# Kernel tuning notes

Hardware: AMD Instinct MI355X
Metric: run time of the kernel (lower is better)

Reference implementation:

```python
import jax, jax.numpy as jnp
import numpy as np

D_MODEL = 512
NUM_HEADS = 8
D_HEAD = D_MODEL // NUM_HEADS
QMAX = 127.0  # int8 narrow-range symmetric
EPS = 1e-8


def _quant_dequant_weight(w):
    # per-output-channel symmetric int8 quant-dequant (brevitas default style)
    s = jnp.maximum(jnp.max(jnp.abs(w), axis=1, keepdims=True) / QMAX, EPS)
    return jnp.clip(jnp.round(w / s), -QMAX, QMAX) * s


def _quant_dequant_act(x):
    # per-tensor symmetric int8 quant-dequant (QuantIdentity)
    s = jnp.maximum(jnp.max(jnp.abs(x)) / QMAX, EPS)
    return jnp.clip(jnp.round(x / s), -QMAX, QMAX) * s


def _qlinear(x, w, b):
    return jnp.einsum('btd,od->bto', x, _quant_dequant_weight(w)) + b


def setup_inputs() -> dict:
    key = jax.random.key(0)
    ks = jax.random.split(key, 10)
    B, T = 2, 4096
    lim = 1.0 / np.sqrt(D_MODEL)
    mk = lambda k: jax.random.uniform(k, (D_MODEL, D_MODEL), jnp.float32, -lim, lim)
    mb = lambda k: jax.random.uniform(k, (D_MODEL,), jnp.float32, -lim, lim)
    return {
        'x': jax.random.normal(ks[0], (B, T, D_MODEL), jnp.float32),
        'mask': jax.random.randint(ks[1], (B, T), 0, 2, jnp.int32),
        'Wq': mk(ks[2]), 'bq': mb(ks[3]),
        'Wk': mk(ks[4]), 'bk': mb(ks[5]),
        'Wv': mk(ks[6]), 'bv': mb(ks[7]),
        'Wo': mk(ks[8]), 'bo': mb(ks[9]),
    }


def reference(x, mask, Wq, bq, Wk, bk, Wv, bv, Wo, bo):
    B, T, _ = x.shape
    shape = lambda t: t.reshape(B, T, NUM_HEADS, D_HEAD).transpose(0, 2, 1, 3)  # (B,H,T,dh)
    q = shape(_qlinear(x, Wq, bq))
    k = shape(_qlinear(x, Wk, bk))
    v = shape(_qlinear(x, Wv, bv))
    scores = jnp.einsum('bhtd,bhsd->bhts', q, k) / np.sqrt(D_HEAD)
    keep = (mask != 0)[:, None, None, :]  # (B,1,1,T), 0 = masked
    scores = jnp.where(keep, scores, -jnp.inf)
    attn = jax.nn.softmax(scores, axis=-1)
    ctx = jnp.einsum('bhts,bhsd->bhtd', attn, v)
    ctx = ctx.transpose(0, 2, 1, 3).reshape(B, T, D_MODEL)
    out = _qlinear(ctx, Wo, bo)
    return _quant_dequant_act(out)
```

## Files before the change

### kernel.cpp

```cpp
#include <hip/hip_runtime.h>
#include <hip/hip_bf16.h>

typedef __bf16 bf16;
typedef __bf16 bf16x8 __attribute__((ext_vector_type(8)));
typedef __bf16 bf16x4v __attribute__((ext_vector_type(4)));
typedef float f32x4 __attribute__((ext_vector_type(4)));

#define D_MODEL 512
#define T_SEQ   4096
#define NH      8
#define DH      64
#define M_ROWS  8192
#define VROW    8224
#define QK_SCALE 0.18033688011112042f

__device__ __forceinline__ void gload16(const void* g, void* l) {
  __builtin_amdgcn_global_load_lds(
      (const __attribute__((address_space(1))) unsigned int*)g,
      (__attribute__((address_space(3))) unsigned int*)l, 16, 0, 0);
}

#define WAITV(N) asm volatile("s_waitcnt vmcnt(" #N ")" ::: "memory")
#define CFENCE   asm volatile("" ::: "memory")

__global__ __launch_bounds__(256) void prep_all(
    const void* __restrict__ x, const int* __restrict__ mask,
    const void* __restrict__ Wq, const void* __restrict__ Wk,
    const void* __restrict__ Wv, const void* __restrict__ Wo,
    const void* __restrict__ bq, const void* __restrict__ bk,
    const void* __restrict__ bv, const void* __restrict__ bo,
    bf16* __restrict__ out, float* __restrict__ bf, float* __restrict__ mf,
    int* __restrict__ flag, unsigned int* __restrict__ amax)
{
  __shared__ int wcnt[4];
  __shared__ int sfl;
  const int tid = threadIdx.x;
  const unsigned short* xr = (const unsigned short*)x;

  int cnt = 0;
  for (int i = tid; i < 4096; i += 256) {
    unsigned short u = xr[i];
    int e = (u >> 7) & 0xFF;
    bool insane = (e >= 133) || (e > 0 && e <= 96) || (e == 0 && (u & 0x7F) != 0);
    cnt += insane ? 1 : 0;
  }
#pragma unroll
  for (int off = 32; off >= 1; off >>= 1) cnt += __shfl_xor(cnt, off);
  if ((tid & 63) == 0) wcnt[tid >> 6] = cnt;
  __syncthreads();
  if (tid == 0) sfl = ((wcnt[0] + wcnt[1] + wcnt[2] + wcnt[3]) > 400) ? 1 : 0;
  __syncthreads();
  const int fl = sfl;

  const int blk = blockIdx.x;
  if (blk < 512) {
    int wave = tid >> 6, lane = tid & 63;
    int gid = blk * 4 + wave;
    int w = gid >> 9, row = gid & 511;
    const void* W = (w == 0) ? Wq : (w == 1) ? Wk : (w == 2) ? Wv : Wo;
    float v[8]; float am = 0.f;
#pragma unroll
    for (int i = 0; i < 8; i++) {
      int idx = row * D_MODEL + lane + 64 * i;
      v[i] = fl ? ((const float*)W)[idx] : (float)((const bf16*)W)[idx];
      am = fmaxf(am, fabsf(v[i]));
    }
#pragma unroll
    for (int off = 32; off >= 1; off >>= 1) am = fmaxf(am, __shfl_xor(am, off));
    float s = fmaxf(am / 127.0f, 1e-8f);
    bf16* dst = out + (size_t)gid * D_MODEL;
#pragma unroll
    for (int i = 0; i < 8; i++) {
      float q = rintf(v[i] / s);
      q = fminf(fmaxf(q, -127.f), 127.f);
      dst[lane + 64 * i] = (bf16)(q * s);
    }
  } else {
    int ab = blk - 512;
    int j = ab * 1024 + tid * 4;
    int4 mv = *(const int4*)&mask[j];
    mf[j + 0] = mv.x ? -16.0f : -1e30f;
    mf[j + 1] = mv.y ? -16.0f : -1e30f;
    mf[j + 2] = mv.z ? -16.0f : -1e30f;
    mf[j + 3] = mv.w ? -16.0f : -1e30f;
    if (ab == 0) {
      const void* ps[4] = {bq, bk, bv, bo};
      for (int t = tid; t < 4 * D_MODEL; t += 256) {
        int w = t >> 9, o = t & 511;
        bf[t] = fl ? ((const float*)ps[w])[o] : (float)((const bf16*)ps[w])[o];
      }
      if (tid == 0) { *flag = fl; *amax = 0u; }
    }
  }
}

__global__ __launch_bounds__(256) void convert_x(const void* __restrict__ xr,
                                                 const int* __restrict__ flag,
                                                 bf16* __restrict__ xb, int n)
{
  int i = (blockIdx.x * blockDim.x + threadIdx.x) * 4;
  if (i >= n) return;
  if (*flag) {
    float4 v = *(const float4*)((const float*)xr + i);
    __align__(8) bf16 o[4] = {(bf16)v.x, (bf16)v.y, (bf16)v.z, (bf16)v.w};
    *(uint2*)(xb + i) = *(uint2*)o;
  } else {
    *(uint2*)(xb + i) = *(const uint2*)((const bf16*)xr + i);
  }
}

__global__ __launch_bounds__(256) void gemm_qkv(
    const bf16* __restrict__ A, const bf16* __restrict__ W,
    const float* __restrict__ bias,
    bf16* __restrict__ Qh, bf16* __restrict__ Kh, bf16* __restrict__ VTP)
{
  __shared__ __align__(16) bf16 As[2][128 * 32];
  __shared__ __align__(16) bf16 Bs[2][128 * 32];

  const int tid = threadIdx.x;
  const int wave = tid >> 6, lane = tid & 63;
  const int lr = lane & 15, quad = lane >> 4;
  const int wm = (wave >> 1) * 64, wn = (wave & 1) * 64;
  const int m0 = blockIdx.x * 128, n0 = blockIdx.y * 128;
  const int sec = blockIdx.y >> 2;

  const bf16* aSrc[2]; const bf16* bSrc[2];
#pragma unroll
  for (int ii = 0; ii < 2; ii++) {
    int s = ii * 256 + tid, row = s >> 2, sl = s & 3;
    int g = (row ^ (row >> 2)) & 3;
    aSrc[ii] = A + (size_t)(m0 + row) * D_MODEL + ((sl ^ g) << 3);
    bSrc[ii] = W + (size_t)(n0 + row) * D_MODEL + ((sl ^ g) << 3);
  }

  f32x4 acc[4][4];
#pragma unroll
  for (int i = 0; i < 4; i++)
#pragma unroll
    for (int j = 0; j < 4; j++) acc[i][j] = f32x4{0.f, 0.f, 0.f, 0.f};

#pragma unroll
  for (int d = 0; d < 2; d++) {
#pragma unroll
    for (int ii = 0; ii < 2; ii++) {
      int s = ii * 256 + tid;
      gload16(aSrc[ii] + d * 32, &As[d][s * 8]);
      gload16(bSrc[ii] + d * 32, &Bs[d][s * 8]);
    }
  }
  WAITV(4);
  __builtin_amdgcn_s_barrier();
  CFENCE;

  for (int k = 0; k < 16; k++) {
    const int cur = k & 1;
    bf16x8 af[4], bfr[4];
#pragma unroll
    for (int mt = 0; mt < 4; mt++) {
      int row = wm + mt * 16 + lr;
      af[mt] = *(const bf16x8*)&As[cur][row * 32 + ((quad ^ ((row ^ (row >> 2)) & 3)) << 3)];
    }
#pragma unroll
    for (int nt = 0; nt < 4; nt++) {
      int row = wn + nt * 16 + lr;
      bfr[nt] = *(const bf16x8*)&Bs[cur][row * 32 + ((quad ^ ((row ^ (row >> 2)) & 3)) << 3)];
    }
    if (sec == 2) {
#pragma unroll
      for (int mt = 0; mt < 4; mt++)
#pragma unroll
        for (int nt = 0; nt < 4; nt++)
          acc[mt][nt] = __builtin_amdgcn_mfma_f32_16x16x32_bf16(af[mt], bfr[nt], acc[mt][nt], 0, 0, 0);
    } else {
#pragma unroll
      for (int mt = 0; mt < 4; mt++)
#pragma unroll
        for (int nt = 0; nt < 4; nt++)
          acc[nt][mt] = __builtin_amdgcn_mfma_f32_16x16x32_bf16(bfr[nt], af[mt], acc[nt][mt], 0, 0, 0);
    }

    if (k < 15) {
      __builtin_amdgcn_s_barrier();
      CFENCE;
      if (k < 14) {
#pragma unroll
        for (int ii = 0; ii < 2; ii++) {
          int s = ii * 256 + tid;
          gload16(aSrc[ii] + (k + 2) * 32, &As[cur][s * 8]);
          gload16(bSrc[ii] + (k + 2) * 32, &Bs[cur][s * 8]);
        }
        WAITV(4);
      } else {
        WAITV(0);
      }
      __builtin_amdgcn_s_barrier();
      CFENCE;
    }
  }

  if (sec == 2) {
#pragma unroll
    for (int mt = 0; mt < 4; mt++) {
      int grow = m0 + wm + mt * 16 + quad * 4;
#pragma unroll
      for (int nt = 0; nt < 4; nt++) {
        int gcol = n0 + wn + nt * 16 + lr;
        float b = bias[gcol];
        bf16x4v pk;
#pragma unroll
        for (int r = 0; r < 4; r++) pk[r] = (bf16)(acc[mt][nt][r] + b);
        *(bf16x4v*)(VTP + (size_t)(gcol - 1024) * VROW + grow) = pk;
      }
    }
  } else {
    const float scale = (sec == 0) ? QK_SCALE : 1.0f;
    bf16* dst = (sec == 0) ? Qh : Kh;
#pragma unroll
    for (int i = 0; i < 4; i++) {
      int cbase = n0 + wn + i * 16 + quad * 4;
      int c = cbase & 511;
      int hh = c >> 6, c64 = c & 63;
      f32x4 bv = *(const f32x4*)&bias[cbase];
#pragma unroll
      for (int j = 0; j < 4; j++) {
        int row = m0 + wm + j * 16 + lr;
        int bb = row >> 12, t = row & 4095;
        bf16x4v pk;
#pragma unroll
        for (int r = 0; r < 4; r++) pk[r] = (bf16)((acc[i][j][r] + bv[r]) * scale);
        *(bf16x4v*)(dst + ((size_t)(bb * NH + hh) * T_SEQ + t) * DH + c64) = pk;
      }
    }
  }
}

__global__ __launch_bounds__(256) void gemm_o(
    const bf16* __restrict__ A, const bf16* __restrict__ W,
    const float* __restrict__ bias,
    float* __restrict__ Cf, unsigned int* __restrict__ amaxp)
{
  __shared__ __align__(16) bf16 As[2][64 * 32];
  __shared__ __align__(16) bf16 Bs[2][128 * 32];
  __shared__ float wred[4];

  const int tid = threadIdx.x;
  const int wave = tid >> 6, lane = tid & 63;
  const int lr = lane & 15, quad = lane >> 4;
  const int wm = (wave >> 1) * 32, wn = (wave & 1) * 64;
  const int m0 = blockIdx.x * 64, n0 = blockIdx.y * 128;

  const bf16* aSrc; const bf16* bSrc[2];
  {
    int s = tid, row = s >> 2, sl = s & 3;
    int g = (row ^ (row >> 2)) & 3;
    aSrc = A + (size_t)(m0 + row) * D_MODEL + ((sl ^ g) << 3);
  }
#pragma unroll
  for (int ii = 0; ii < 2; ii++) {
    int s = ii * 256 + tid, row = s >> 2, sl = s & 3;
    int g = (row ^ (row >> 2)) & 3;
    bSrc[ii] = W + (size_t)(n0 + row) * D_MODEL + ((sl ^ g) << 3);
  }

  f32x4 acc[2][4];
#pragma unroll
  for (int i = 0; i < 2; i++)
#pragma unroll
    for (int j = 0; j < 4; j++) acc[i][j] = f32x4{0.f, 0.f, 0.f, 0.f};

#pragma unroll
  for (int d = 0; d < 2; d++) {
    gload16(aSrc + d * 32, &As[d][tid * 8]);
#pragma unroll
    for (int ii = 0; ii < 2; ii++) {
      int s = ii * 256 + tid;
      gload16(bSrc[ii] + d * 32, &Bs[d][s * 8]);
    }
  }
  WAITV(3);
  __builtin_amdgcn_s_barrier();
  CFENCE;

  for (int k = 0; k < 16; k++) {
    const int cur = k & 1;
    bf16x8 af[2], bfr[4];
#pragma unroll
    for (int mt = 0; mt < 2; mt++) {
      int row = wm + mt * 16 + lr;
      af[mt] = *(const bf16x8*)&As[cur][row * 32 + ((quad ^ ((row ^ (row >> 2)) & 3)) << 3)];
    }
#pragma unroll
    for (int nt = 0; nt < 4; nt++) {
      int row = wn + nt * 16 + lr;
      bfr[nt] = *(const bf16x8*)&Bs[cur][row * 32 + ((quad ^ ((row ^ (row >> 2)) & 3)) << 3)];
    }
#pragma unroll
    for (int mt = 0; mt < 2; mt++)
#pragma unroll
      for (int nt = 0; nt < 4; nt++)
        acc[mt][nt] = __builtin_amdgcn_mfma_f32_16x16x32_bf16(af[mt], bfr[nt], acc[mt][nt], 0, 0, 0);

    if (k < 15) {
      __builtin_amdgcn_s_barrier();
      CFENCE;
      if (k < 14) {
        gload16(aSrc + (k + 2) * 32, &As[cur][tid * 8]);
#pragma unroll
        for (int ii = 0; ii < 2; ii++) {
          int s = ii * 256 + tid;
          gload16(bSrc[ii] + (k + 2) * 32, &Bs[cur][s * 8]);
        }
        WAITV(3);
      } else {
        WAITV(0);
      }
      __builtin_amdgcn_s_barrier();
      CFENCE;
    }
  }

  float lmax = 0.f;
#pragma unroll
  for (int mt = 0; mt < 2; mt++) {
    int grow = m0 + wm + mt * 16 + quad * 4;
#pragma unroll
    for (int nt = 0; nt < 4; nt++) {
      int gcol = n0 + wn + nt * 16 + lr;
      float b = bias[gcol];
#pragma unroll
      for (int r = 0; r < 4; r++) {
        float v = acc[mt][nt][r] + b;
        Cf[(size_t)(grow + r) * D_MODEL + gcol] = v;
        lmax = fmaxf(lmax, fabsf(v));
      }
    }
  }
#pragma unroll
  for (int off = 32; off >= 1; off >>= 1) lmax = fmaxf(lmax, __shfl_xor(lmax, off));
  if (lane == 0) wred[wave] = lmax;
  __syncthreads();
  if (tid == 0) {
    float m = fmaxf(fmaxf(wred[0], wred[1]), fmaxf(wred[2], wred[3]));
    atomicMax(amaxp, __float_as_uint(m));
  }
}

__global__ __launch_bounds__(256, 2) void attn(
    const bf16* __restrict__ Q, const bf16* __restrict__ K, const bf16* __restrict__ VT,
    const float* __restrict__ maskf, bf16* __restrict__ ctx)
{
  __shared__ __align__(16) bf16 Ks[3][64 * 64];
  __shared__ __align__(16) bf16 Vs[3][64 * 64];
  __shared__ __align__(16) float Mf[T_SEQ];

  const int tid = threadIdx.x;
  const int wave = tid >> 6, lane = tid & 63;
  const int lr = lane & 15, quad = lane >> 4;
  const int i = blockIdx.x;
  const int bh = (i & 7) * 2 + ((i >> 3) & 1);
  const int qb = i >> 4;
  const int b = bh >> 3, h = bh & 7;
  const int q0 = qb * 128 + wave * 32;

  const bf16* Qb = Q + (size_t)bh * T_SEQ * DH;
  const bf16* Kb = K + (size_t)bh * T_SEQ * DH;
  const bf16* Vb = VT + (size_t)(h * DH) * VROW + (size_t)b * T_SEQ;
  const float* mb = maskf + b * T_SEQ;

  const int phase = (qb * 2) & 63;

  const bf16* kSrc[2]; const bf16* vSrc[2];
#pragma unroll
  for (int ii = 0; ii < 2; ii++) {
    int s = ii * 256 + tid, row = s >> 3, sl = s & 7;
    int kt = row >> 4, m = row & 15;
    int keym = ((m >> 2) << 3) + ((kt & 1) << 2) + (m & 3) + ((kt >> 1) << 5);
    kSrc[ii] = Kb + (size_t)keym * DH + ((sl ^ (row & 7)) << 3);
    vSrc[ii] = Vb + (size_t)row * VROW + ((sl ^ (row & 7)) << 3);
  }

  bf16x8 qf[2][2];
#pragma unroll
  for (int qt = 0; qt < 2; qt++) {
    const bf16* rq = Qb + (size_t)(q0 + qt * 16 + lr) * DH;
    qf[qt][0] = *(const bf16x8*)(rq + quad * 8);
    qf[qt][1] = *(const bf16x8*)(rq + 32 + quad * 8);
  }
  WAITV(0);

#pragma unroll
  for (int ii = 0; ii < 4; ii++) {
    int g = ii * 256 + tid;
    gload16(mb + g * 4, &Mf[g * 4]);
  }
#pragma unroll
  for (int d = 0; d < 3; d++) {
    int kb = ((phase + d) & 63) * 64;
#pragma unroll
    for (int ii = 0; ii < 2; ii++) {
      int s = ii * 256 + tid;
      gload16(kSrc[ii] + (size_t)kb * DH, &Ks[d][s * 8]);
      gload16(vSrc[ii] + kb, &Vs[d][s * 8]);
    }
  }

  f32x4 O[2][4];
#pragma unroll
  for (int a = 0; a < 2; a++)
#pragma unroll
    for (int c = 0; c < 4; c++) O[a][c] = f32x4{0.f, 0.f, 0.f, 0.f};
  float lacc[2] = {0.f, 0.f};

  WAITV(8);
  __builtin_amdgcn_s_barrier();
  CFENCE;

  int cur = 0, cc = phase;
  for (int j = 0; j < 64; j++) {
    f32x4 mk[4];
#pragma unroll
    for (int kt = 0; kt < 4; kt++)
      mk[kt] = *(const f32x4*)&Mf[cc * 64 + ((kt >> 1) << 5) + (quad << 3) + ((kt & 1) << 2)];

    bf16x8 kr[4][2];
#pragma unroll
    for (int kt = 0; kt < 4; kt++)
#pragma unroll
      for (int kh = 0; kh < 2; kh++)
        kr[kt][kh] = *(const bf16x8*)&Ks[cur][(kt * 16 + lr) * 64 +
                                             (((kh * 4 + quad) ^ (lr & 7)) << 3)];

    bf16x8 pfa[2][2];
#pragma unroll
    for (int qt = 0; qt < 2; qt++) {
      f32x4 z[4];
#pragma unroll
      for (int kt = 0; kt < 4; kt++) {
        f32x4 t = mk[kt];
        t = __builtin_amdgcn_mfma_f32_16x16x32_bf16(kr[kt][0], qf[qt][0], t, 0, 0, 0);
        t = __builtin_amdgcn_mfma_f32_16x16x32_bf16(kr[kt][1], qf[qt][1], t, 0, 0, 0);
        z[kt] = t;
      }
      float la = lacc[qt];
#pragma unroll
      for (int kt = 0; kt < 4; kt++) {
#pragma unroll
        for (int r = 0; r < 4; r++) {
          float p = __builtin_amdgcn_exp2f(z[kt][r]);
          la += p;
          pfa[qt][kt >> 1][((kt & 1) << 2) + r] = (bf16)p;
        }
      }
      lacc[qt] = la;
    }

    bf16x8 vr[4][2];
#pragma unroll
    for (int nt = 0; nt < 4; nt++)
#pragma unroll
      for (int ks = 0; ks < 2; ks++)
        vr[nt][ks] = *(const bf16x8*)&Vs[cur][(nt * 16 + lr) * 64 +
                                             (((ks * 4 + quad) ^ (lr & 7)) << 3)];

#pragma unroll
    for (int nt = 0; nt < 4; nt++)
#pragma unroll
      for (int qt = 0; qt < 2; qt++) {
        O[qt][nt] = __builtin_amdgcn_mfma_f32_16x16x32_bf16(pfa[qt][0], vr[nt][0], O[qt][nt], 0, 0, 0);
        O[qt][nt] = __builtin_amdgcn_mfma_f32_16x16x32_bf16(pfa[qt][1], vr[nt][1], O[qt][nt], 0, 0, 0);
      }

    if (j < 63) {
      __builtin_amdgcn_s_barrier();
      CFENCE;
      if (j < 61) {
        int kb = ((cc + 3) & 63) * 64;
#pragma unroll
        for (int ii = 0; ii < 2; ii++) {
          int s = ii * 256 + tid;
          gload16(kSrc[ii] + (size_t)kb * DH, &Ks[cur][s * 8]);
          gload16(vSrc[ii] + kb, &Vs[cur][s * 8]);
        }
        WAITV(8);
      } else if (j == 61) {
        WAITV(4);
      } else {
        WAITV(0);
      }
      __builtin_amdgcn_s_barrier();
      CFENCE;
    }
    cur = (cur == 2) ? 0 : cur + 1;
    cc = (cc + 1) & 63;
  }

#pragma unroll
  for (int qt = 0; qt < 2; qt++) {
    float ls = lacc[qt];
    ls += __shfl_xor(ls, 16);
    ls += __shfl_xor(ls, 32);
    float linv = 1.0f / ls;
    float lO[4];
#pragma unroll
    for (int r = 0; r < 4; r++) lO[r] = __shfl(linv, quad * 4 + r);
#pragma unroll
    for (int nt = 0; nt < 4; nt++)
#pragma unroll
      for (int r = 0; r < 4; r++) {
        size_t row = (size_t)(b * T_SEQ + q0 + qt * 16 + quad * 4 + r);
        ctx[row * D_MODEL + h * DH + nt * 16 + lr] = (bf16)(O[qt][nt][r] * lO[r]);
      }
  }
}

__global__ __launch_bounds__(256) void act_qdq(
    const float* __restrict__ pre, const unsigned int* __restrict__ amaxp,
    const int* __restrict__ flag, void* __restrict__ outv, int n)
{
  int i = (blockIdx.x * blockDim.x + threadIdx.x) * 4;
  if (i >= n) return;
  float s = fmaxf(__uint_as_float(*amaxp) / 127.0f, 1e-8f);
  float4 v = *(const float4*)(pre + i);
  float o[4] = {v.x, v.y, v.z, v.w};
#pragma unroll
  for (int r = 0; r < 4; r++) {
    float q = rintf(o[r] / s);
    q = fminf(fmaxf(q, -127.f), 127.f);
    o[r] = q * s;
  }
  if (*flag) {
    *(float4*)((float*)outv + i) = make_float4(o[0], o[1], o[2], o[3]);
  } else {
    __align__(8) bf16 ob[4] = {(bf16)o[0], (bf16)o[1], (bf16)o[2], (bf16)o[3]};
    *(uint2*)((bf16*)outv + i) = *(uint2*)ob;
  }
}

extern "C" void kernel_launch(void* const* d_in, const int* in_sizes, int n_in,
                              void* d_out, int out_size, void* d_ws, size_t ws_size,
                              hipStream_t stream) {
  const void* x    = d_in[0];
  const int*  mask = (const int*)d_in[1];
  const void* Wq = d_in[2]; const void* bq = d_in[3];
  const void* Wk = d_in[4]; const void* bk = d_in[5];
  const void* Wv = d_in[6]; const void* bv = d_in[7];
  const void* Wo = d_in[8]; const void* bo = d_in[9];

  char* ws = (char*)d_ws;
  int*  flag  = (int*)(ws + 0);
  unsigned int* amax = (unsigned int*)(ws + 64);
  float* biasf = (float*)(ws + 1024);
  float* maskf = (float*)(ws + 16384);
  bf16* Wt  = (bf16*)(ws + 65536);
  bf16* xb  = (bf16*)(ws + 4194304);
  bf16* Qm  = (bf16*)(ws + 12582912);
  bf16* Km  = (bf16*)(ws + 20971520);
  bf16* VT  = (bf16*)(ws + 29360128);
  bf16* Cm  = (bf16*)(ws + 4194304);
  float* pre = (float*)(ws + 12582912);

  prep_all<<<520, 256, 0, stream>>>(x, mask, Wq, Wk, Wv, Wo, bq, bk, bv, bo,
                                    Wt, biasf, maskf, flag, amax);
  convert_x<<<4096, 256, 0, stream>>>(x, flag, xb, M_ROWS * D_MODEL);
  gemm_qkv<<<dim3(64, 12), 256, 0, stream>>>(xb, Wt, biasf, Qm, Km, VT);
  attn<<<512, 256, 0, stream>>>(Qm, Km, VT, maskf, Cm);
  gemm_o<<<dim3(128, 4), 256, 0, stream>>>(Cm, Wt + 3*262144, biasf + 1536, pre, amax);
  act_qdq<<<4096, 256, 0, stream>>>(pre, amax, flag, d_out, M_ROWS * D_MODEL);
}
```

Baseline: 219.4 us.

## Fuse output activation quant into gemm_o via grid-wide amax barrier

Removes the separate act_qdq kernel and the fp32 pre-activation round trip. gemm_o keeps results in registers, publishes its block amax, then spins on a global counter until all 512 blocks are done before quantizing and writing the output directly. convert_x now returns early when the input is already bf16, and gemm_qkv reads the raw input in that case. The spin barrier assumes all 512 blocks are co-resident (launch bounds raised to 2 waves per SIMD); if they are not, the kernel deadlocks. The output stores are scalar rather than vectorized.

```diff
diff --git a/kernel.cpp b/kernel.cpp
--- a/kernel.cpp
+++ b/kernel.cpp
@@ -30,7 +30,8 @@
     const void* __restrict__ bq, const void* __restrict__ bk,
     const void* __restrict__ bv, const void* __restrict__ bo,
     bf16* __restrict__ out, float* __restrict__ bf, float* __restrict__ mf,
-    int* __restrict__ flag, unsigned int* __restrict__ amax)
+    int* __restrict__ flag, unsigned int* __restrict__ amax,
+    int* __restrict__ done)
 {
   __shared__ int wcnt[4];
   __shared__ int sfl;
@@ -89,7 +90,7 @@
         int w = t >> 9, o = t & 511;
         bf[t] = fl ? ((const float*)ps[w])[o] : (float)((const bf16*)ps[w])[o];
       }
-      if (tid == 0) { *flag = fl; *amax = 0u; }
+      if (tid == 0) { *flag = fl; *amax = 0u; *done = 0; }
     }
   }
 }
@@ -98,19 +99,17 @@
                                                  const int* __restrict__ flag,
                                                  bf16* __restrict__ xb, int n)
 {
+  if (*flag == 0) return;
   int i = (blockIdx.x * blockDim.x + threadIdx.x) * 4;
   if (i >= n) return;
-  if (*flag) {
-    float4 v = *(const float4*)((const float*)xr + i);
-    __align__(8) bf16 o[4] = {(bf16)v.x, (bf16)v.y, (bf16)v.z, (bf16)v.w};
-    *(uint2*)(xb + i) = *(uint2*)o;
-  } else {
-    *(uint2*)(xb + i) = *(const uint2*)((const bf16*)xr + i);
-  }
+  float4 v = *(const float4*)((const float*)xr + i);
+  __align__(8) bf16 o[4] = {(bf16)v.x, (bf16)v.y, (bf16)v.z, (bf16)v.w};
+  *(uint2*)(xb + i) = *(uint2*)o;
 }
 
 __global__ __launch_bounds__(256) void gemm_qkv(
-    const bf16* __restrict__ A, const bf16* __restrict__ W,
+    const void* __restrict__ xraw, const bf16* __restrict__ xb,
+    const int* __restrict__ flag, const bf16* __restrict__ W,
     const float* __restrict__ bias,
     bf16* __restrict__ Qh, bf16* __restrict__ Kh, bf16* __restrict__ VTP)
 {
@@ -123,6 +122,8 @@
   const int wm = (wave >> 1) * 64, wn = (wave & 1) * 64;
   const int m0 = blockIdx.x * 128, n0 = blockIdx.y * 128;
   const int sec = blockIdx.y >> 2;
+
+  const bf16* A = (*flag) ? xb : (const bf16*)xraw;
 
   const bf16* aSrc[2]; const bf16* bSrc[2];
 #pragma unroll
@@ -234,14 +235,16 @@
   }
 }
 
-__global__ __launch_bounds__(256) void gemm_o(
+__global__ __launch_bounds__(256, 2) void gemm_o(
     const bf16* __restrict__ A, const bf16* __restrict__ W,
-    const float* __restrict__ bias,
-    float* __restrict__ Cf, unsigned int* __restrict__ amaxp)
+    const float* __restrict__ bias, const int* __restrict__ flag,
+    unsigned int* __restrict__ amaxp, int* __restrict__ done,
+    void* __restrict__ outv)
 {
   __shared__ __align__(16) bf16 As[2][64 * 32];
   __shared__ __align__(16) bf16 Bs[2][128 * 32];
   __shared__ float wred[4];
+  __shared__ float ssc;
 
   const int tid = threadIdx.x;
   const int wave = tid >> 6, lane = tid & 63;
@@ -321,8 +324,7 @@
 
   float lmax = 0.f;
 #pragma unroll
-  for (int mt = 0; mt < 2; mt++) {
-    int grow = m0 + wm + mt * 16 + quad * 4;
+  for (int mt = 0; mt < 2; mt++)
 #pragma unroll
     for (int nt = 0; nt < 4; nt++) {
       int gcol = n0 + wn + nt * 16 + lr;
@@ -330,18 +332,45 @@
 #pragma unroll
       for (int r = 0; r < 4; r++) {
         float v = acc[mt][nt][r] + b;
-        Cf[(size_t)(grow + r) * D_MODEL + gcol] = v;
+        acc[mt][nt][r] = v;
         lmax = fmaxf(lmax, fabsf(v));
       }
     }
-  }
 #pragma unroll
   for (int off = 32; off >= 1; off >>= 1) lmax = fmaxf(lmax, __shfl_xor(lmax, off));
   if (lane == 0) wred[wave] = lmax;
   __syncthreads();
+
   if (tid == 0) {
     float m = fmaxf(fmaxf(wred[0], wred[1]), fmaxf(wred[2], wred[3]));
     atomicMax(amaxp, __float_as_uint(m));
+    __threadfence();
+    atomicAdd(done, 1);
+    while (atomicAdd(done, 0) < 512) __builtin_amdgcn_s_sleep(8);
+    __threadfence();
+    unsigned int a = atomicMax(amaxp, 0u);
+    ssc = fmaxf(__uint_as_float(a) / 127.0f, 1e-8f);
+  }
+  __syncthreads();
+  const float s = ssc;
+  const int fl = *flag;
+
+#pragma unroll
+  for (int mt = 0; mt < 2; mt++) {
+    int grow = m0 + wm + mt * 16 + quad * 4;
+#pragma unroll
+    for (int nt = 0; nt < 4; nt++) {
+      int gcol = n0 + wn + nt * 16 + lr;
+#pragma unroll
+      for (int r = 0; r < 4; r++) {
+        float q = rintf(acc[mt][nt][r] / s);
+        q = fminf(fmaxf(q, -127.f), 127.f);
+        float o = q * s;
+        size_t idx = (size_t)(grow + r) * D_MODEL + gcol;
+        if (fl) ((float*)outv)[idx] = o;
+        else    ((bf16*)outv)[idx] = (bf16)o;
+      }
+    }
   }
 }
 
@@ -513,29 +542,6 @@
   }
 }
 
-__global__ __launch_bounds__(256) void act_qdq(
-    const float* __restrict__ pre, const unsigned int* __restrict__ amaxp,
-    const int* __restrict__ flag, void* __restrict__ outv, int n)
-{
-  int i = (blockIdx.x * blockDim.x + threadIdx.x) * 4;
-  if (i >= n) return;
-  float s = fmaxf(__uint_as_float(*amaxp) / 127.0f, 1e-8f);
-  float4 v = *(const float4*)(pre + i);
-  float o[4] = {v.x, v.y, v.z, v.w};
-#pragma unroll
-  for (int r = 0; r < 4; r++) {
-    float q = rintf(o[r] / s);
-    q = fminf(fmaxf(q, -127.f), 127.f);
-    o[r] = q * s;
-  }
-  if (*flag) {
-    *(float4*)((float*)outv + i) = make_float4(o[0], o[1], o[2], o[3]);
-  } else {
-    __align__(8) bf16 ob[4] = {(bf16)o[0], (bf16)o[1], (bf16)o[2], (bf16)o[3]};
-    *(uint2*)((bf16*)outv + i) = *(uint2*)ob;
-  }
-}
-
 extern "C" void kernel_launch(void* const* d_in, const int* in_sizes, int n_in,
                               void* d_out, int out_size, void* d_ws, size_t ws_size,
                               hipStream_t stream) {
@@ -549,6 +555,7 @@
   char* ws = (char*)d_ws;
   int*  flag  = (int*)(ws + 0);
   unsigned int* amax = (unsigned int*)(ws + 64);
+  int*  done  = (int*)(ws + 128);
   float* biasf = (float*)(ws + 1024);
   float* maskf = (float*)(ws + 16384);
   bf16* Wt  = (bf16*)(ws + 65536);
@@ -556,14 +563,14 @@
   bf16* Qm  = (bf16*)(ws + 12582912);
   bf16* Km  = (bf16*)(ws + 20971520);
   bf16* VT  = (bf16*)(ws + 29360128);
-  bf16* Cm  = (bf16*)(ws + 4194304);
-  float* pre = (float*)(ws + 12582912);
+  bf16* Cm  = (bf16*)(ws + 4194304 + 8388608 - 4194304);
+  Cm = (bf16*)(ws + 46137344);
 
   prep_all<<<520, 256, 0, stream>>>(x, mask, Wq, Wk, Wv, Wo, bq, bk, bv, bo,
-                                    Wt, biasf, maskf, flag, amax);
+                                    Wt, biasf, maskf, flag, amax, done);
   convert_x<<<4096, 256, 0, stream>>>(x, flag, xb, M_ROWS * D_MODEL);
-  gemm_qkv<<<dim3(64, 12), 256, 0, stream>>>(xb, Wt, biasf, Qm, Km, VT);
+  gemm_qkv<<<dim3(64, 12), 256, 0, stream>>>(x, xb, flag, Wt, biasf, Qm, Km, VT);
   attn<<<512, 256, 0, stream>>>(Qm, Km, VT, maskf, Cm);
-  gemm_o<<<dim3(128, 4), 256, 0, stream>>>(Cm, Wt + 3*262144, biasf + 1536, pre, amax);
-  act_qdq<<<4096, 256, 0, stream>>>(pre, amax, flag, d_out, M_ROWS * D_MODEL);
-}
+  gemm_o<<<dim3(128, 4), 256, 0, stream>>>(Cm, Wt + 3*262144, biasf + 1536,
+                                           flag, amax, done, d_out);
+}
```

New measurement: 242.0 us. +10.3%, slower.
